# Performance work log

Hardware: AMD Instinct MI355X
Metric: run time of the kernel (lower is better)

## Reference

```python
import jax, jax.numpy as jnp
import numpy as np

WH, WW = 8, 8          # window height/width
NH = 8                 # num heads
DIM = 256              # channels
B_ = 512               # num_windows * batch
N = WH * WW            # tokens per window
HD = DIM // NH         # head dim


def _rel_constants():
    # log-spaced continuous relative coords table (Swin-V2 CPB input)
    ch = np.arange(-(WH - 1), WH, dtype=np.float32) / (WH - 1)
    cw = np.arange(-(WW - 1), WW, dtype=np.float32) / (WW - 1)
    table = np.stack(np.meshgrid(ch, cw, indexing='ij'), axis=-1)[None] * 8.0  # [1,2WH-1,2WW-1,2]
    table = np.sign(table) * np.log2(np.abs(table) + 1.0) / np.log2(8.0)
    # relative position index
    coords = np.stack(np.meshgrid(np.arange(WH), np.arange(WW), indexing='ij'))
    cf = coords.reshape(2, -1)
    rel = (cf[:, :, None] - cf[:, None, :]).transpose(1, 2, 0).astype(np.int64)
    rel[..., 0] += WH - 1
    rel[..., 1] += WW - 1
    rel[..., 0] *= 2 * WW - 1
    idx = rel.sum(-1)  # [N,N]
    return jnp.asarray(table, dtype=jnp.float32), jnp.asarray(idx)

TABLE, IDX = _rel_constants()


def setup_inputs() -> dict:
    key = jax.random.key(0)
    ks = jax.random.split(key, 16)
    s = lambda k, shape, sc=0.02: (jax.random.normal(k, shape, dtype=jnp.float32) * sc)
    inp = {
        'x1': jax.random.normal(ks[0], (B_, N, DIM), dtype=jnp.float32),
        'x2': jax.random.normal(ks[1], (B_, N, DIM), dtype=jnp.float32),
        'qkv_w1': s(ks[2], (3 * DIM, DIM)),
        'q_bias_1': jnp.zeros((DIM,), jnp.float32),
        'v_bias_1': jnp.zeros((DIM,), jnp.float32),
        'proj_w1': s(ks[3], (DIM, DIM)),
        'proj_b1': jnp.zeros((DIM,), jnp.float32),
        'logit_scale_1': jnp.log(10.0) * jnp.ones((NH, 1, 1), jnp.float32),
        'cpb1_w1': s(ks[4], (512, 2), 0.1),
        'cpb1_b1': jnp.zeros((512,), jnp.float32),
        'cpb1_w2': s(ks[5], (NH, 512), 0.1),
        'pc1_w': s(ks[6], (NH, 2 * NH), 0.1),
        'pc1_b': jnp.zeros((NH,), jnp.float32),
        'qkv_w2': s(ks[7], (3 * DIM, DIM)),
        'q_bias_2': jnp.zeros((DIM,), jnp.float32),
        'v_bias_2': jnp.zeros((DIM,), jnp.float32),
        'proj_w2': s(ks[8], (DIM, DIM)),
        'proj_b2': jnp.zeros((DIM,), jnp.float32),
        'logit_scale_2': jnp.log(10.0) * jnp.ones((NH, 1, 1), jnp.float32),
        'cpb2_w1': s(ks[9], (512, 2), 0.1),
        'cpb2_b1': jnp.zeros((512,), jnp.float32),
        'cpb2_w2': s(ks[10], (NH, 512), 0.1),
        'pc2_w': s(ks[11], (NH, 2 * NH), 0.1),
        'pc2_b': jnp.zeros((NH,), jnp.float32),
    }
    return inp


def _qkv(x, w, qb, vb):
    b = jnp.concatenate([qb, jnp.zeros_like(vb), vb])
    y = (x @ w.T + b).reshape(x.shape[0], N, 3, NH, HD).transpose(2, 0, 3, 1, 4)
    return y[0], y[1], y[2]  # each [B_, NH, N, HD]


def _l2norm(t):
    n = jnp.linalg.norm(t, axis=-1, keepdims=True)
    return t / jnp.maximum(n, 1e-12)


def _view(qn, k_same_n, k_diff_n, v, logit_scale, pc_w, pc_b, cw1, cb1, cw2, proj_w, proj_b):
    same = jnp.einsum('bhnd,bhmd->bhnm', qn, k_same_n)
    diff = jnp.einsum('bhnd,bhmd->bhnm', qn, k_diff_n)
    cat = jnp.concatenate([same, diff], axis=1).transpose(0, 2, 3, 1)  # [B,N,N,2H]
    scale = jnp.exp(jnp.minimum(logit_scale, jnp.log(100.0)))  # clamp at 1/0.01
    attn = (cat @ pc_w.T + pc_b).transpose(0, 3, 1, 2) * scale  # [B,H,N,N]
    # CPB MLP -> bias table -> gather
    tbl = (jax.nn.relu(TABLE @ cw1.T + cb1) @ cw2.T).reshape(-1, NH)  # [(2WH-1)*(2WW-1), H]
    bias = tbl[IDX.reshape(-1)].reshape(N, N, NH).transpose(2, 0, 1)  # [H,N,N]
    attn = attn + (16.0 * jax.nn.sigmoid(bias))[None]
    attn = jax.nn.softmax(attn, axis=-1)
    out = jnp.einsum('bhnm,bhmd->bhnd', attn, v).transpose(0, 2, 1, 3).reshape(-1, N, DIM)
    return out @ proj_w.T + proj_b


def reference(x1, x2, qkv_w1, q_bias_1, v_bias_1, proj_w1, proj_b1, logit_scale_1,
              cpb1_w1, cpb1_b1, cpb1_w2, pc1_w, pc1_b,
              qkv_w2, q_bias_2, v_bias_2, proj_w2, proj_b2, logit_scale_2,
              cpb2_w1, cpb2_b1, cpb2_w2, pc2_w, pc2_b):
    q1, k1, v1 = _qkv(x1, qkv_w1, q_bias_1, v_bias_1)
    q2, k2, v2 = _qkv(x2, qkv_w2, q_bias_2, v_bias_2)
    q1n, k1n = _l2norm(q1), _l2norm(k1)
    q2n, k2n = _l2norm(q2), _l2norm(k2)
    o1 = _view(q1n, k1n, k2n, v1, logit_scale_1, pc1_w, pc1_b, cpb1_w1, cpb1_b1, cpb1_w2, proj_w1, proj_b1)
    o2 = _view(q2n, k2n, k1n, v2, logit_scale_2, pc2_w, pc2_b, cpb2_w1, cpb2_b1, cpb2_w2, proj_w2, proj_b2)
    return o1, o2
```

## Files before the change

kernel.cpp:

```cpp
#include <hip/hip_runtime.h>

typedef _Float16 f16;
typedef f16  f16x8  __attribute__((ext_vector_type(8)));
typedef f16  f16x4v __attribute__((ext_vector_type(4)));
typedef f16  f16x2  __attribute__((ext_vector_type(2)));
typedef float f32x4 __attribute__((ext_vector_type(4)));

#define MFMA_F16(a,b,c) __builtin_amdgcn_mfma_f32_16x16x32_f16((a),(b),(c),0,0,0)

#define NWIN 512
#define SB_QST 3088
#define SB_KST 48
#define BUFX_ST 264
#define BUFO_HEAD 2304
#define VT_ST 72
#define STBL_STRIDE 9
#define SM_BYTES 70656
#define STBL_OFF 49408

__device__ __forceinline__ f16x8 ld_f16x8(const float* __restrict__ p) {
  f32x4 a = *(const f32x4*)p;
  f32x4 b = *(const f32x4*)(p + 4);
  f16x8 r;
  r[0] = (f16)a[0]; r[1] = (f16)a[1]; r[2] = (f16)a[2]; r[3] = (f16)a[3];
  r[4] = (f16)b[0]; r[5] = (f16)b[1]; r[6] = (f16)b[2]; r[7] = (f16)b[3];
  return r;
}

__global__ __launch_bounds__(256) void prep_all(
    const float* __restrict__ w1a, const float* __restrict__ b1a,
    const float* __restrict__ w2a,
    const float* __restrict__ w1b, const float* __restrict__ b1b,
    const float* __restrict__ w2b,
    const float* __restrict__ qkvw1, const float* __restrict__ qkvw2,
    const float* __restrict__ pw1, const float* __restrict__ pw2,
    float* __restrict__ sg16,
    f16* __restrict__ wq1f, f16* __restrict__ wq2f,
    f16* __restrict__ pw1f, f16* __restrict__ pw2f) {
  const int b = blockIdx.x;
  if (b >= 450) {
    const int cb = b - 450;
    const float* src; f16* dst; int base;
    if (cb < 96)       { src = qkvw1; dst = wq1f; base = cb * 2048; }
    else if (cb < 192) { src = qkvw2; dst = wq2f; base = (cb - 96) * 2048; }
    else if (cb < 224) { src = pw1;   dst = pw1f; base = (cb - 192) * 2048; }
    else               { src = pw2;   dst = pw2f; base = (cb - 224) * 2048; }
    const int o = base + threadIdx.x * 8;
    *(f16x8*)(dst + o) = ld_f16x8(src + o);
    return;
  }
  const int view = b / 225;
  const int e    = b % 225;
  const float* __restrict__ w1 = view ? w1b : w1a;
  const float* __restrict__ b1 = view ? b1b : b1a;
  const float* __restrict__ w2 = view ? w2b : w2a;
  const int t = threadIdx.x;
  const int i = e / 15, j = e % 15;
  const float vi = 8.0f * (float)(i - 7) * (1.0f / 7.0f);
  const float vj = 8.0f * (float)(j - 7) * (1.0f / 7.0f);
  const float in0 = copysignf(log2f(fabsf(vi) + 1.0f) * (1.0f / 3.0f), vi);
  const float in1 = copysignf(log2f(fabsf(vj) + 1.0f) * (1.0f / 3.0f), vj);
  float acc[8] = {0.f,0.f,0.f,0.f,0.f,0.f,0.f,0.f};
#pragma unroll
  for (int uu = 0; uu < 2; ++uu) {
    const int u = t + uu * 256;
    float hv = fmaxf(w1[2*u] * in0 + w1[2*u+1] * in1 + b1[u], 0.0f);
#pragma unroll
    for (int hh = 0; hh < 8; ++hh) acc[hh] += w2[hh*512 + u] * hv;
  }
#pragma unroll
  for (int off = 32; off >= 1; off >>= 1)
#pragma unroll
    for (int hh = 0; hh < 8; ++hh) acc[hh] += __shfl_xor(acc[hh], off, 64);
  __shared__ float red[4][8];
  if ((t & 63) == 0) {
#pragma unroll
    for (int hh = 0; hh < 8; ++hh) red[t >> 6][hh] = acc[hh];
  }
  __syncthreads();
  if (t < 8) {
    float s = red[0][t] + red[1][t] + red[2][t] + red[3][t];
    sg16[(view * 225 + e) * 8 + t] = 16.0f / (1.0f + __expf(-s));
  }
}

__global__ __launch_bounds__(512, 2) void fused_attn(
    const float* __restrict__ x1, const float* __restrict__ x2,
    const f16* __restrict__ qkvw1, const float* __restrict__ qb1, const float* __restrict__ vb1,
    const f16* __restrict__ qkvw2, const float* __restrict__ qb2, const float* __restrict__ vb2,
    const float* __restrict__ pcw1, const float* __restrict__ pcb1, const float* __restrict__ ls1,
    const float* __restrict__ pcw2, const float* __restrict__ pcb2, const float* __restrict__ ls2,
    const f16* __restrict__ pw1, const float* __restrict__ pb1,
    const f16* __restrict__ pw2, const float* __restrict__ pb2,
    const float* __restrict__ sg16,
    float* __restrict__ outp) {
  const int win = blockIdx.x;
  const int tid = threadIdx.x;
  const int lane = tid & 63, h = tid >> 6;
  const int quad = lane >> 4, m = lane & 15;

  __shared__ __align__(16) char sm[SM_BYTES];
  f16* bufX  = (f16*)sm;
  f16* bufO  = (f16*)(sm + 33792);
  char* Sbc  = sm;
  f16* preB  = (f16*)sm;
  float* sTbl = (float*)(sm + STBL_OFF);

  const f32x4 z4 = {0.f, 0.f, 0.f, 0.f};
  f16x8 aqF[2][4], kfF[2][4], bvF[2][2][2];
  f16* oh = bufO + h * BUFO_HEAD;

  for (int view = 0; view < 2; ++view) {
    const float* __restrict__ xv = (view ? x2 : x1) + (size_t)win * (64 * 256);
    const f16* __restrict__ W    = view ? qkvw2 : qkvw1;
    const float* __restrict__ qb = view ? qb2 : qb1;
    const float* __restrict__ vb = view ? vb2 : vb1;

    __syncthreads();
    for (int i = tid; i < 2048; i += 512) {
      const int row = i >> 5, c8 = i & 31;
      *(f16x8*)(bufX + row * BUFX_ST + c8 * 8) = ld_f16x8(xv + row * 256 + c8 * 8);
    }
    __syncthreads();

    for (int sec = 0; sec < 3; ++sec) {
      f32x4 acc0[4], acc1[4];
#pragma unroll
      for (int t = 0; t < 4; ++t) { acc0[t] = z4; acc1[t] = z4; }
      const f16* wb = W + (size_t)(sec * 256 + h * 32) * 256 + quad * 8;
      __builtin_amdgcn_s_setprio(1);
#pragma unroll 2
      for (int k8 = 0; k8 < 8; ++k8) {
        f16x8 a0 = *(const f16x8*)(wb + (size_t)m * 256 + k8 * 32);
        f16x8 a1 = *(const f16x8*)(wb + (size_t)(16 + m) * 256 + k8 * 32);
#pragma unroll
        for (int tt = 0; tt < 4; ++tt) {
          f16x8 bfr = *(const f16x8*)(bufX + (tt * 16 + m) * BUFX_ST + k8 * 32 + quad * 8);
          acc0[tt] = MFMA_F16(a0, bfr, acc0[tt]);
          acc1[tt] = MFMA_F16(a1, bfr, acc1[tt]);
        }
      }
      __builtin_amdgcn_s_setprio(0);
      float bs0[4], bs1[4];
#pragma unroll
      for (int r = 0; r < 4; ++r) {
        int c0 = h * 32 + quad * 4 + r;
        bs0[r] = (sec == 0) ? qb[c0] : (sec == 2 ? vb[c0] : 0.f);
        bs1[r] = (sec == 0) ? qb[c0 + 16] : (sec == 2 ? vb[c0 + 16] : 0.f);
      }
#pragma unroll
      for (int tt = 0; tt < 4; ++tt) {
        float v0[4], v1[4];
#pragma unroll
        for (int r = 0; r < 4; ++r) { v0[r] = acc0[tt][r] + bs0[r]; v1[r] = acc1[tt][r] + bs1[r]; }
        if (sec < 2) {
          float ss = 0.f;
#pragma unroll
          for (int r = 0; r < 4; ++r) ss += v0[r] * v0[r] + v1[r] * v1[r];
          ss += __shfl_xor(ss, 16, 64);
          ss += __shfl_xor(ss, 32, 64);
          float s = 1.0f / fmaxf(sqrtf(ss), 1e-12f);
#pragma unroll
          for (int r = 0; r < 4; ++r) { v0[r] *= s; v1[r] *= s; }
        }
        const int n = tt * 16 + m;
        if (sec < 2) {
          f16x4v p0, p1;
#pragma unroll
          for (int r = 0; r < 4; ++r) { p0[r] = (f16)v0[r]; p1[r] = (f16)v1[r]; }
          char* ob = (char*)oh;
          const int sw = (n & 7) << 4;
          *(f16x4v*)(ob + ((n * 64 + quad * 8) ^ sw))      = p0;
          *(f16x4v*)(ob + ((n * 64 + 32 + quad * 8) ^ sw)) = p1;
        } else {
#pragma unroll
          for (int r = 0; r < 4; ++r) {
            oh[(quad * 4 + r) * VT_ST + n]      = (f16)v0[r];
            oh[(quad * 4 + 16 + r) * VT_ST + n] = (f16)v1[r];
          }
        }
      }
      if (sec == 0) {
#pragma unroll
        for (int rt = 0; rt < 4; ++rt) {
          const int n = rt * 16 + m;
          aqF[view][rt] = *(const f16x8*)((char*)oh + ((n * 64 + quad * 16) ^ ((n & 7) << 4)));
        }
      } else if (sec == 1) {
#pragma unroll
        for (int ct = 0; ct < 4; ++ct) {
          const int n = ct * 16 + m;
          kfF[view][ct] = *(const f16x8*)((char*)oh + ((n * 64 + quad * 16) ^ ((n & 7) << 4)));
        }
      } else {
#pragma unroll
        for (int nt = 0; nt < 2; ++nt)
#pragma unroll
          for (int kv = 0; kv < 2; ++kv)
            bvF[view][nt][kv] = *(const f16x8*)(oh + (nt * 16 + m) * VT_ST + kv * 32 + quad * 8);
      }
    }
  }
  __syncthreads();

  for (int i = tid; i < 3600; i += 512)
    sTbl[(i >> 3) * STBL_STRIDE + (i & 7)] = sg16[i];

#pragma unroll
  for (int view = 0; view < 2; ++view) {
    const float* __restrict__ pcw = view ? pcw2 : pcw1;
    f16x2 w0[4], w1[4];
#pragma unroll
    for (int c = 0; c < 4; ++c) {
      f16x2 a, b;
      a[0] = (f16)pcw[h * 16 + c];     a[1] = (f16)pcw[h * 16 + 8 + c];
      b[0] = (f16)pcw[h * 16 + 4 + c]; b[1] = (f16)pcw[h * 16 + 12 + c];
      w0[c] = a; w1[c] = b;
    }
    const float pcb_h = (view ? pcb2 : pcb1)[h];
    const float lsv = (view ? ls2 : ls1)[h];
    const float scale_h = __expf(fminf(lsv, 4.6051702f));
    const float pcbs = pcb_h * scale_h;
    const float* tblv = sTbl + view * (225 * STBL_STRIDE);

    f32x4 oacc[4][2];
#pragma unroll
    for (int rt = 0; rt < 4; ++rt) {
      f16x8 aq = aqF[view][rt];
      __builtin_amdgcn_s_setprio(1);
#pragma unroll
      for (int ct = 0; ct < 4; ++ct) {
        const int kk = ct * 16 + m;
        const int wbase = kk * SB_KST + (h << 2);
        f32x4 Ss = MFMA_F16(aq, kfF[view][ct], z4);
        f32x4 Sd = MFMA_F16(aq, kfF[1 - view][ct], z4);
#pragma unroll
        for (int r = 0; r < 4; ++r) {
          f16x2 pr; pr[0] = (f16)Ss[r]; pr[1] = (f16)Sd[r];
          *(f16x2*)(Sbc + (quad * 4 + r) * SB_QST + wbase) = pr;
        }
      }
      __builtin_amdgcn_s_setprio(0);
      __syncthreads();

      const int n = rt * 16 + m;
      const int nh_ = n >> 3, nw_ = n & 7;
      const int rbase = m * SB_QST;
      float logit[16];
#pragma unroll
      for (int j = 0; j < 16; ++j) {
        const int mm = (j < 8) ? (quad * 8 + j) : (32 + quad * 8 + (j - 8));
        const int b0 = rbase + mm * SB_KST;
        f16x8 s0 = *(const f16x8*)(Sbc + b0);
        f16x8 s1 = *(const f16x8*)(Sbc + b0 + 16);
        const f16x2* s0p = (const f16x2*)&s0;
        const f16x2* s1p = (const f16x2*)&s1;
        float mix = 0.f;
#pragma unroll
        for (int c = 0; c < 4; ++c) {
          mix = __builtin_amdgcn_fdot2(s0p[c], w0[c], mix, false);
          mix = __builtin_amdgcn_fdot2(s1p[c], w1[c], mix, false);
        }
        const int idx = (nh_ - (mm >> 3) + 7) * 15 + (nw_ - (mm & 7) + 7);
        logit[j] = mix * scale_h + pcbs + tblv[idx * STBL_STRIDE + h];
      }
      float mx = -1e30f;
#pragma unroll
      for (int j = 0; j < 16; ++j) mx = fmaxf(mx, logit[j]);
      mx = fmaxf(mx, __shfl_xor(mx, 16, 64));
      mx = fmaxf(mx, __shfl_xor(mx, 32, 64));
      float p[16], sum = 0.f;
#pragma unroll
      for (int j = 0; j < 16; ++j) { p[j] = __expf(logit[j] - mx); sum += p[j]; }
      sum += __shfl_xor(sum, 16, 64);
      sum += __shfl_xor(sum, 32, 64);
      float inv = 1.0f / sum;
      f16x8 av0, av1;
#pragma unroll
      for (int j = 0; j < 8; ++j) { av0[j] = (f16)(p[j] * inv); av1[j] = (f16)(p[8 + j] * inv); }
      __builtin_amdgcn_s_setprio(1);
#pragma unroll
      for (int nt = 0; nt < 2; ++nt) {
        f32x4 z = z4;
        z = MFMA_F16(av0, bvF[view][nt][0], z);
        z = MFMA_F16(av1, bvF[view][nt][1], z);
        oacc[rt][nt] = z;
      }
      __builtin_amdgcn_s_setprio(0);
      __syncthreads();
    }

#pragma unroll
    for (int mt = 0; mt < 4; ++mt)
#pragma unroll
      for (int nt = 0; nt < 2; ++nt)
#pragma unroll
        for (int r = 0; r < 4; ++r)
          preB[(mt * 16 + quad * 4 + r) * 264 + h * 32 + nt * 16 + m] = (f16)oacc[mt][nt][r];
    __syncthreads();

    const f16* __restrict__ Wp = view ? pw2 : pw1;
    const float* __restrict__ pb = view ? pb2 : pb1;
    f32x4 pacc0[4], pacc1[4];
#pragma unroll
    for (int t = 0; t < 4; ++t) { pacc0[t] = z4; pacc1[t] = z4; }
    __builtin_amdgcn_s_setprio(1);
#pragma unroll 2
    for (int ks = 0; ks < 8; ++ks) {
      f16x8 pa0 = *(const f16x8*)(Wp + (size_t)(h * 32 + m) * 256 + ks * 32 + quad * 8);
      f16x8 pa1 = *(const f16x8*)(Wp + (size_t)(h * 32 + 16 + m) * 256 + ks * 32 + quad * 8);
#pragma unroll
      for (int tt = 0; tt < 4; ++tt) {
        f16x8 bfr = *(const f16x8*)(preB + (tt * 16 + m) * 264 + ks * 32 + quad * 8);
        pacc0[tt] = MFMA_F16(pa0, bfr, pacc0[tt]);
        pacc1[tt] = MFMA_F16(pa1, bfr, pacc1[tt]);
      }
    }
    __builtin_amdgcn_s_setprio(0);
    float* obase = outp + (size_t)(view * NWIN + win) * (64 * 256);
#pragma unroll
    for (int tt = 0; tt < 4; ++tt) {
      f32x4 p0, p1;
#pragma unroll
      for (int r = 0; r < 4; ++r) {
        p0[r] = pacc0[tt][r] + pb[h * 32 + quad * 4 + r];
        p1[r] = pacc1[tt][r] + pb[h * 32 + 16 + quad * 4 + r];
      }
      const int n = tt * 16 + m;
      *(f32x4*)(obase + n * 256 + h * 32 + quad * 4)      = p0;
      *(f32x4*)(obase + n * 256 + h * 32 + 16 + quad * 4) = p1;
    }
    __syncthreads();
  }
}

extern "C" void kernel_launch(void* const* d_in, const int* in_sizes, int n_in,
                              void* d_out, int out_size, void* d_ws, size_t ws_size,
                              hipStream_t stream) {
  (void)in_sizes; (void)n_in; (void)out_size; (void)ws_size;
  const float* x1   = (const float*)d_in[0];
  const float* x2   = (const float*)d_in[1];
  const float* qkvw1= (const float*)d_in[2];
  const float* qb1  = (const float*)d_in[3];
  const float* vb1  = (const float*)d_in[4];
  const float* pw1  = (const float*)d_in[5];
  const float* pb1  = (const float*)d_in[6];
  const float* ls1  = (const float*)d_in[7];
  const float* cw11 = (const float*)d_in[8];
  const float* cb11 = (const float*)d_in[9];
  const float* cw12 = (const float*)d_in[10];
  const float* pcw1 = (const float*)d_in[11];
  const float* pcb1 = (const float*)d_in[12];
  const float* qkvw2= (const float*)d_in[13];
  const float* qb2  = (const float*)d_in[14];
  const float* vb2  = (const float*)d_in[15];
  const float* pw2  = (const float*)d_in[16];
  const float* pb2  = (const float*)d_in[17];
  const float* ls2  = (const float*)d_in[18];
  const float* cw21 = (const float*)d_in[19];
  const float* cb21 = (const float*)d_in[20];
  const float* cw22 = (const float*)d_in[21];
  const float* pcw2 = (const float*)d_in[22];
  const float* pcb2 = (const float*)d_in[23];

  float* SG16 = (float*)d_ws;
  f16* wq1f = (f16*)((char*)d_ws + 14400);
  f16* wq2f = wq1f + 196608;
  f16* pw1f = wq2f + 196608;
  f16* pw2f = pw1f + 65536;
  float* out = (float*)d_out;

  prep_all<<<706, 256, 0, stream>>>(cw11, cb11, cw12, cw21, cb21, cw22,
                                    qkvw1, qkvw2, pw1, pw2,
                                    SG16, wq1f, wq2f, pw1f, pw2f);
  fused_attn<<<NWIN, 512, 0, stream>>>(x1, x2,
      wq1f, qb1, vb1, wq2f, qb2, vb2,
      pcw1, pcb1, ls1, pcw2, pcb2, ls2,
      pw1f, pb1, pw2f, pb2, SG16, out);
}
```

Baseline: 273.9 us.

## Process two row tiles per barrier phase with swizzled score buffer and head-major bias table

The score/mix loop now handles two 16-row query tiles per phase, cutting the __syncthreads count per view in half. The shared score buffer drops padding and uses an XOR swizzle on the key index to avoid bank conflicts. The CPB bias table is transposed to a head-major layout so each head reads a contiguous row. Shared memory use rises (SM_BYTES grows), which may lower occupancy.

After: 281.0 us. +2.6%, slower.

```diff
diff --git a/kernel.cpp b/kernel.cpp
--- a/kernel.cpp
+++ b/kernel.cpp
@@ -9,14 +9,12 @@
 #define MFMA_F16(a,b,c) __builtin_amdgcn_mfma_f32_16x16x32_f16((a),(b),(c),0,0,0)
 
 #define NWIN 512
-#define SB_QST 3088
-#define SB_KST 48
+#define SB_QST 2064
 #define BUFX_ST 264
 #define BUFO_HEAD 2304
 #define VT_ST 72
-#define STBL_STRIDE 9
-#define SM_BYTES 70656
-#define STBL_OFF 49408
+#define SM_BYTES 80512
+#define STBL_OFF 66048
 
 __device__ __forceinline__ f16x8 ld_f16x8(const float* __restrict__ p) {
   f32x4 a = *(const f32x4*)p;
@@ -203,8 +201,10 @@
   }
   __syncthreads();
 
-  for (int i = tid; i < 3600; i += 512)
-    sTbl[(i >> 3) * STBL_STRIDE + (i & 7)] = sg16[i];
+  for (int i = tid; i < 3600; i += 512) {
+    const int v_ = i / 1800, rem = i % 1800;
+    sTbl[v_ * 1808 + (rem & 7) * 226 + (rem >> 3)] = sg16[i];
+  }
 
 #pragma unroll
   for (int view = 0; view < 2; ++view) {
@@ -221,72 +221,81 @@
     const float lsv = (view ? ls2 : ls1)[h];
     const float scale_h = __expf(fminf(lsv, 4.6051702f));
     const float pcbs = pcb_h * scale_h;
-    const float* tblv = sTbl + view * (225 * STBL_STRIDE);
+    const float* tblv = sTbl + view * 1808 + h * 226;
 
     f32x4 oacc[4][2];
 #pragma unroll
-    for (int rt = 0; rt < 4; ++rt) {
-      f16x8 aq = aqF[view][rt];
+    for (int c = 0; c < 2; ++c) {
       __builtin_amdgcn_s_setprio(1);
 #pragma unroll
-      for (int ct = 0; ct < 4; ++ct) {
-        const int kk = ct * 16 + m;
-        const int wbase = kk * SB_KST + (h << 2);
-        f32x4 Ss = MFMA_F16(aq, kfF[view][ct], z4);
-        f32x4 Sd = MFMA_F16(aq, kfF[1 - view][ct], z4);
-#pragma unroll
-        for (int r = 0; r < 4; ++r) {
-          f16x2 pr; pr[0] = (f16)Ss[r]; pr[1] = (f16)Sd[r];
-          *(f16x2*)(Sbc + (quad * 4 + r) * SB_QST + wbase) = pr;
+      for (int rtp = 0; rtp < 2; ++rtp) {
+        f16x8 aq = aqF[view][2 * c + rtp];
+#pragma unroll
+        for (int ct = 0; ct < 4; ++ct) {
+          const int kk = ct * 16 + m;
+          f32x4 Ss = MFMA_F16(aq, kfF[view][ct], z4);
+          f32x4 Sd = MFMA_F16(aq, kfF[1 - view][ct], z4);
+#pragma unroll
+          for (int r = 0; r < 4; ++r) {
+            const int qrow = rtp * 16 + quad * 4 + r;
+            const int sw = (quad * 4 + r) & 7;
+            f16x2 pr; pr[0] = (f16)Ss[r]; pr[1] = (f16)Sd[r];
+            *(f16x2*)(Sbc + qrow * SB_QST + ((kk ^ sw) << 5) + (h << 2)) = pr;
+          }
         }
       }
       __builtin_amdgcn_s_setprio(0);
       __syncthreads();
 
-      const int n = rt * 16 + m;
-      const int nh_ = n >> 3, nw_ = n & 7;
-      const int rbase = m * SB_QST;
-      float logit[16];
-#pragma unroll
-      for (int j = 0; j < 16; ++j) {
-        const int mm = (j < 8) ? (quad * 8 + j) : (32 + quad * 8 + (j - 8));
-        const int b0 = rbase + mm * SB_KST;
-        f16x8 s0 = *(const f16x8*)(Sbc + b0);
-        f16x8 s1 = *(const f16x8*)(Sbc + b0 + 16);
-        const f16x2* s0p = (const f16x2*)&s0;
-        const f16x2* s1p = (const f16x2*)&s1;
-        float mix = 0.f;
-#pragma unroll
-        for (int c = 0; c < 4; ++c) {
-          mix = __builtin_amdgcn_fdot2(s0p[c], w0[c], mix, false);
-          mix = __builtin_amdgcn_fdot2(s1p[c], w1[c], mix, false);
-        }
-        const int idx = (nh_ - (mm >> 3) + 7) * 15 + (nw_ - (mm & 7) + 7);
-        logit[j] = mix * scale_h + pcbs + tblv[idx * STBL_STRIDE + h];
-      }
-      float mx = -1e30f;
-#pragma unroll
-      for (int j = 0; j < 16; ++j) mx = fmaxf(mx, logit[j]);
-      mx = fmaxf(mx, __shfl_xor(mx, 16, 64));
-      mx = fmaxf(mx, __shfl_xor(mx, 32, 64));
-      float p[16], sum = 0.f;
-#pragma unroll
-      for (int j = 0; j < 16; ++j) { p[j] = __expf(logit[j] - mx); sum += p[j]; }
-      sum += __shfl_xor(sum, 16, 64);
-      sum += __shfl_xor(sum, 32, 64);
-      float inv = 1.0f / sum;
-      f16x8 av0, av1;
-#pragma unroll
-      for (int j = 0; j < 8; ++j) { av0[j] = (f16)(p[j] * inv); av1[j] = (f16)(p[8 + j] * inv); }
-      __builtin_amdgcn_s_setprio(1);
-#pragma unroll
-      for (int nt = 0; nt < 2; ++nt) {
-        f32x4 z = z4;
-        z = MFMA_F16(av0, bvF[view][nt][0], z);
-        z = MFMA_F16(av1, bvF[view][nt][1], z);
-        oacc[rt][nt] = z;
-      }
-      __builtin_amdgcn_s_setprio(0);
+#pragma unroll
+      for (int rtp = 0; rtp < 2; ++rtp) {
+        const int rt = 2 * c + rtp;
+        const int n = rt * 16 + m;
+        const int nh_ = n >> 3, nw_ = n & 7;
+        const int rbase = (rtp * 16 + m) * SB_QST;
+        const int swr = m & 7;
+        float logit[16];
+#pragma unroll
+        for (int j = 0; j < 16; ++j) {
+          const int mm = (j < 8) ? (quad * 8 + j) : (32 + quad * 8 + (j - 8));
+          const int b0 = rbase + ((mm ^ swr) << 5);
+          f16x8 s0 = *(const f16x8*)(Sbc + b0);
+          f16x8 s1 = *(const f16x8*)(Sbc + b0 + 16);
+          const f16x2* s0p = (const f16x2*)&s0;
+          const f16x2* s1p = (const f16x2*)&s1;
+          float mix = 0.f;
+#pragma unroll
+          for (int cc = 0; cc < 4; ++cc) {
+            mix = __builtin_amdgcn_fdot2(s0p[cc], w0[cc], mix, false);
+            mix = __builtin_amdgcn_fdot2(s1p[cc], w1[cc], mix, false);
+          }
+          const int idx = (nh_ - (mm >> 3) + 7) * 15 + (nw_ - (mm & 7) + 7);
+          logit[j] = mix * scale_h + pcbs + tblv[idx];
+        }
+        float mx = -1e30f;
+#pragma unroll
+        for (int j = 0; j < 16; ++j) mx = fmaxf(mx, logit[j]);
+        mx = fmaxf(mx, __shfl_xor(mx, 16, 64));
+        mx = fmaxf(mx, __shfl_xor(mx, 32, 64));
+        float p[16], sum = 0.f;
+#pragma unroll
+        for (int j = 0; j < 16; ++j) { p[j] = __expf(logit[j] - mx); sum += p[j]; }
+        sum += __shfl_xor(sum, 16, 64);
+        sum += __shfl_xor(sum, 32, 64);
+        float inv = 1.0f / sum;
+        f16x8 av0, av1;
+#pragma unroll
+        for (int j = 0; j < 8; ++j) { av0[j] = (f16)(p[j] * inv); av1[j] = (f16)(p[8 + j] * inv); }
+        __builtin_amdgcn_s_setprio(1);
+#pragma unroll
+        for (int nt = 0; nt < 2; ++nt) {
+          f32x4 z = z4;
+          z = MFMA_F16(av0, bvF[view][nt][0], z);
+          z = MFMA_F16(av1, bvF[view][nt][1], z);
+          oacc[rt][nt] = z;
+        }
+        __builtin_amdgcn_s_setprio(0);
+      }
       __syncthreads();
     }
 
```
